# Performance work log

Measured on AMD Instinct MI355X. Metric: run time of the kernel, lower is better.

Reference implementation:

```python
import jax, jax.numpy as jnp
import numpy as np

C = 512
NC = 12
EPS = 1e-5

ADJ = np.array([
    [0,0,0,1,0,1,1,1,1,1,1,1],
    [0,0,0,1,0,1,1,1,1,1,1,1],
    [0,0,0,1,0,1,1,1,1,1,1,1],
    [1,1,1,0,1,1,1,1,1,1,1,1],
    [0,0,0,1,0,1,1,1,1,1,1,1],
    [1,1,1,1,1,0,1,1,1,0,0,0],
    [1,1,1,1,1,1,0,0,0,1,1,1],
    [1,1,1,1,1,1,0,0,0,1,1,1],
    [1,1,1,1,1,1,0,0,0,1,1,1],
    [1,1,1,1,1,0,1,1,1,0,0,0],
    [1,1,1,1,1,0,1,1,1,0,0,0],
    [1,1,1,1,1,0,1,1,1,0,0,0]], dtype=np.float32)
# per-AU region selection: 0=up,1=mid,2=down1,3=down2 (AU1,2,4 up; AU6 mid; AU7 up; AU10 d2; AU12,14,15 d1; AU17,23,24 d2)
SEL = np.array([0,0,0,1,0,3,2,2,2,3,3,3])


def setup_inputs() -> dict:
    key = jax.random.key(0)
    ks = jax.random.split(key, 12)
    B, T = 32, 32
    BT = B * T
    s = (2.0 / C) ** 0.5
    return {
        'x': jax.random.normal(ks[0], (BT, 49, C), jnp.float32),
        'adj_mask': jnp.ones((BT, NC, NC), jnp.float32),
        'region_W': jax.random.normal(ks[1], (4, C, C), jnp.float32) * s,
        'region_b': jnp.zeros((4, C), jnp.float32),
        'region_gamma': jnp.ones((4, C), jnp.float32),
        'region_beta': jnp.zeros((4, C), jnp.float32),
        'upfc_W': jax.random.normal(ks[2], (C, 16), jnp.float32) * 0.02,
        'upfc_b': jnp.zeros((16,), jnp.float32),
        'midfc_W': jax.random.normal(ks[3], (C, 2), jnp.float32) * 0.02,
        'midfc_b': jnp.zeros((2,), jnp.float32),
        'd1fc_W': jax.random.normal(ks[4], (C, 8), jnp.float32) * 0.02,
        'd1fc_b': jnp.zeros((8,), jnp.float32),
        'd2fc_W': jax.random.normal(ks[5], (C, 16), jnp.float32) * 0.02,
        'd2fc_b': jnp.zeros((16,), jnp.float32),
        'class_W': jax.random.normal(ks[6], (NC, C, C), jnp.float32) * s,
        'class_b': jnp.zeros((NC, C), jnp.float32),
        'class_gamma': jnp.ones((NC, C), jnp.float32),
        'class_beta': jnp.zeros((NC, C), jnp.float32),
        'gat_W': jax.random.normal(ks[7], (C, C), jnp.float32) * 0.02,
        'gat_al': jax.random.normal(ks[8], (C,), jnp.float32) * 0.02,
        'gat_ar': jax.random.normal(ks[9], (C,), jnp.float32) * 0.02,
        'tconv_W': jax.random.normal(ks[10], (NC, C, 5), jnp.float32) * 0.1,
        'tconv_b': jnp.zeros((NC, C), jnp.float32),
        'tbn_gamma': jnp.ones((NC,), jnp.float32),
        'tbn_beta': jnp.zeros((NC,), jnp.float32),
        'B': B,
        'T': T,
    }


def _bn(x, gamma, beta, axes):
    # training-mode batch norm: stats over `axes`, affine per remaining channel
    mean = x.mean(axes, keepdims=True)
    var = x.var(axes, keepdims=True)
    return gamma * (x - mean) * jax.lax.rsqrt(var + EPS) + beta


def reference(x, adj_mask, region_W, region_b, region_gamma, region_beta,
              upfc_W, upfc_b, midfc_W, midfc_b, d1fc_W, d1fc_b, d2fc_W, d2fc_b,
              class_W, class_b, class_gamma, class_beta,
              gat_W, gat_al, gat_ar, tconv_W, tconv_b, tbn_gamma, tbn_beta, B, T):
    BT = x.shape[0]
    xg = x.reshape(BT, 7, 7, C)
    x_up = xg[:, :3].reshape(BT, 21, C)
    x_mid = xg[:, 2:5].reshape(BT, 21, C)
    x_down = xg[:, 4:].reshape(BT, 21, C)
    # 4 region LinearBlocks (fc -> BN over (batch,seq) per channel -> relu), batched
    regions = jnp.stack([x_up, x_mid, x_down, x_down])  # [4,BT,21,C]
    h = jnp.einsum('rbsc,rcd->rbsd', regions, region_W) + region_b[:, None, None, :]
    h = jax.nn.relu(_bn(h, region_gamma[:, None, None, :], region_beta[:, None, None, :], (1, 2)))
    up_pred = h[0].mean(1) @ upfc_W + upfc_b
    mid_pred = h[1].mean(1) @ midfc_W + midfc_b
    d1_pred = h[2].mean(1) @ d1fc_W + d1fc_b
    d2_pred = h[3].mean(1) @ d2fc_W + d2fc_b
    # 12 per-AU LinearBlocks, batched over the class dim
    cls_in = h[jnp.asarray(SEL)]  # [12,BT,21,C]
    y = jnp.einsum('nbsc,ncd->nbsd', cls_in, class_W) + class_b[:, None, None, :]
    y = jax.nn.relu(_bn(y, class_gamma[:, None, None, :], class_beta[:, None, None, :], (1, 2)))
    f_v = y.mean(2).transpose(1, 0, 2)  # [BT,12,C]
    # cross-region single-head GAT over the fixed 12-node graph, residual, thred=0.1
    adj = jnp.asarray(ADJ)[None] * adj_mask + jnp.eye(NC, dtype=x.dtype)
    hg = f_v @ gat_W  # [BT,12,C]
    e = jax.nn.leaky_relu((hg @ gat_al)[:, :, None] + (hg @ gat_ar)[:, None, :], 0.2)
    attn = jax.nn.softmax(jnp.where(adj > 0.1, e, -1e9), axis=-1)
    g = jnp.einsum('bij,bjc->bic', attn, hg) + f_v
    # per-class depthwise temporal Conv1d (k=5, pad=2, groups=C), batched over classes
    x4 = g.reshape(B, T, NC, C)
    xp = jnp.pad(x4, ((0, 0), (2, 2), (0, 0), (0, 0)))
    v = sum(xp[:, k:k + T] * tconv_W[None, None, :, :, k] for k in range(5)) + tconv_b[None, None]
    v = v.reshape(BT, NC, C)
    out = jax.nn.relu(_bn(v, tbn_gamma[None, :, None], tbn_beta[None, :, None], (0, 2)))
    return (up_pred, mid_pred, d1_pred, d2_pred, out)
```

## Files before the change

### kernel.cpp

```cpp
#include <hip/hip_runtime.h>
#include <hip/hip_bf16.h>

typedef unsigned short u16;
typedef __attribute__((ext_vector_type(8))) __bf16 bf16x8;
typedef __attribute__((ext_vector_type(8))) u16 u16x8;
typedef __attribute__((ext_vector_type(4))) float floatx4;

#define C_     512
#define NC_    12
#define BT_    1024
#define SEQ_   21
#define M_REG  21504
#define M_GAT  12288

__device__ __forceinline__ float bf2f(u16 u) {
  unsigned int v = ((unsigned int)u) << 16;
  float f; __builtin_memcpy(&f, &v, 4); return f;
}
__device__ __forceinline__ u16 f2bf(float f) {
  unsigned int b; __builtin_memcpy(&b, &f, 4);
  unsigned int r = (b + 0x7FFFu + ((b >> 16) & 1u)) >> 16;
  return (u16)r;
}
__device__ __forceinline__ float ldf(const void* p, size_t i, int f32) {
  return f32 ? ((const float*)p)[i] : bf2f(((const u16*)p)[i]);
}
__device__ __forceinline__ u16 ldbf(const void* p, size_t i, int f32) {
  return f32 ? f2bf(((const float*)p)[i]) : ((const u16*)p)[i];
}
__device__ __forceinline__ void stout(void* p, size_t i, float v, int f32) {
  if (f32) ((float*)p)[i] = v; else ((u16*)p)[i] = f2bf(v);
}

typedef __attribute__((address_space(1))) unsigned int as1_u32;
typedef __attribute__((address_space(3))) unsigned int as3_u32;
__device__ __forceinline__ void gl2lds16(const void* g, void* l) {
  __builtin_amdgcn_global_load_lds((const as1_u32*)g, (as3_u32*)l, 16, 0, 0);
}

__global__ void sent_k(float* __restrict__ o, float val) {
  const int i = blockIdx.x * 256 + threadIdx.x;
  if (i < 16384) o[i] = val;
}

__global__ void detect_k(const u16* __restrict__ x, int* __restrict__ flag) {
  __shared__ int cnt;
  if (threadIdx.x == 0) cnt = 0;
  __syncthreads();
  int bad = 0;
  for (int i = threadIdx.x; i < 4096; i += 256) {
    const float v = bf2f(x[i]);
    const float a = fabsf(v);
    if (!(a <= 1e4f)) bad++;
    else if (a > 0.f && a < 1e-35f) bad++;
  }
  atomicAdd(&cnt, bad);
  __syncthreads();
  if (threadIdx.x == 0) *flag = (cnt > 400) ? 1 : 0;
}

__global__ void zero_stats(float* __restrict__ p, int n) {
  const int id = blockIdx.x * 256 + threadIdx.x;
  if (id < n) p[id] = 0.f;
}

__global__ void transpose512(const void* __restrict__ rW, const void* __restrict__ cW,
                             const void* __restrict__ gW, u16* __restrict__ oR,
                             u16* __restrict__ oC, u16* __restrict__ oG,
                             const int* __restrict__ flagp) {
  const int f32 = *flagp;
  const int z = blockIdx.z;
  const void* src; u16* dst; size_t sofs = 0;
  if (z < 4)       { src = rW; sofs = (size_t)z*262144;     dst = oR + (size_t)z*262144; }
  else if (z < 16) { src = cW; sofs = (size_t)(z-4)*262144; dst = oC + (size_t)(z-4)*262144; }
  else             { src = gW;                              dst = oG; }
  __shared__ u16 t[32][33];
  const int tx = threadIdx.x;
  const int cy = blockIdx.y * 32, dx = blockIdx.x * 32;
  for (int i = threadIdx.y; i < 32; i += 8)
    t[i][tx] = ldbf(src, sofs + (size_t)(cy + i)*512 + dx + tx, f32);
  __syncthreads();
  for (int i = threadIdx.y; i < 32; i += 8)
    dst[(size_t)(dx + i)*512 + cy + tx] = t[tx][i];
}

template<int MODE>
__global__ __launch_bounds__(256)
void gemm_k(const void* __restrict__ Abase, const u16* __restrict__ Wtb,
            const void* __restrict__ biasb, u16* __restrict__ outb,
            float* __restrict__ ssumb, float* __restrict__ ssqb,
            const int* __restrict__ flagp, int pk, int n0)
{
  const int f32 = *flagp;
  const int z = blockIdx.z;
  const int zeff = (MODE == 1) ? (n0 + z) : z;
  const void* A = Abase;
  if (MODE == 1) A = (const void*)((const u16*)Abase +
        (size_t)((pk >> (zeff * 2)) & 3) * ((size_t)M_REG * C_));
  const u16* Wt = Wtb + (size_t)zeff * C_ * C_;
  u16* Out = outb + (size_t)z * (size_t)M_REG * C_;

  __shared__ __align__(16) u16 smem[64 * 132];
  u16* As = smem;
  u16* Bs = smem + 4096;

  const int tid  = threadIdx.x;
  const int w    = tid >> 6;
  const int lane = tid & 63;
  const int wm   = w >> 1, wn = w & 1;
  const int r16  = lane & 15, q = lane >> 4;

  const int band = (MODE == 2) ? 12 : 21;
  const int lin  = blockIdx.x;
  const int xcd  = lin & 7;
  const int idx  = lin >> 3;
  const int mi   = xcd * band + idx % band;
  const int ni   = idx / band;
  const int m0   = mi * 128;
  const int nn0  = ni * 128;

  const int sub = lane >> 2;
  const int kq  = (lane & 3) * 8;
  const int am0 = m0 + w*32 + sub;
  const int am1 = am0 + 16;
  long ga0, ga1;
  if (MODE == 0) {
    const int roff = (pk >> (z * 8)) & 0xFF;
    int q21 = am0 / 21; int rm = am0 - q21*21;
    ga0 = (long)q21*49 + roff + rm;
    q21 = am1 / 21; rm = am1 - q21*21;
    ga1 = (long)q21*49 + roff + rm;
  } else { ga0 = am0; ga1 = am1; }
  const size_t aOff0 = (size_t)ga0 * C_ + kq;
  const size_t aOff1 = (size_t)ga1 * C_ + kq;
  const u16* bSrc0 = Wt + (size_t)(nn0 + w*32 + sub) * C_ + kq;
  const u16* bSrc1 = bSrc0 + (size_t)16 * C_;
  u16* aDstW0 = &As[(w*32 +  0) * 32];
  u16* aDstW1 = &As[(w*32 + 16) * 32];
  u16* bDstW0 = &Bs[(w*32 +  0) * 32];
  u16* bDstW1 = &Bs[(w*32 + 16) * 32];
  u16x8* aLds0 = (u16x8*)&As[(w*32 + sub +  0) * 32 + kq];
  u16x8* aLds1 = (u16x8*)&As[(w*32 + sub + 16) * 32 + kq];

  floatx4 acc[4][4];
  #pragma unroll
  for (int i = 0; i < 4; i++)
    #pragma unroll
    for (int j = 0; j < 4; j++)
      acc[i][j] = (floatx4){0.f, 0.f, 0.f, 0.f};

  for (int kk = 0; kk < C_; kk += 32) {
    if (MODE == 0 && f32) {
      const float* p0 = (const float*)A + aOff0 + kk;
      const float* p1 = (const float*)A + aOff1 + kk;
      const floatx4 f00 = *(const floatx4*)p0;
      const floatx4 f01 = *(const floatx4*)(p0 + 4);
      const floatx4 f10 = *(const floatx4*)p1;
      const floatx4 f11 = *(const floatx4*)(p1 + 4);
      u16x8 va0, va1;
      #pragma unroll
      for (int j = 0; j < 4; j++) {
        va0[j] = f2bf(f00[j]); va0[4+j] = f2bf(f01[j]);
        va1[j] = f2bf(f10[j]); va1[4+j] = f2bf(f11[j]);
      }
      __syncthreads();
      gl2lds16(bSrc0, bDstW0); gl2lds16(bSrc1, bDstW1);
      *aLds0 = va0; *aLds1 = va1;
      __syncthreads();
    } else {
      __syncthreads();
      gl2lds16((const u16*)A + aOff0 + kk, aDstW0);
      gl2lds16((const u16*)A + aOff1 + kk, aDstW1);
      gl2lds16(bSrc0, bDstW0);
      gl2lds16(bSrc1, bDstW1);
      __syncthreads();
    }
    bSrc0 += 32; bSrc1 += 32;
    bf16x8 av[4], bv[4];
    #pragma unroll
    for (int mt = 0; mt < 4; mt++)
      av[mt] = *(const bf16x8*)&As[(wm*64 + mt*16 + r16)*32 + q*8];
    #pragma unroll
    for (int nt = 0; nt < 4; nt++)
      bv[nt] = *(const bf16x8*)&Bs[(wn*64 + nt*16 + r16)*32 + q*8];
    #pragma unroll
    for (int mt = 0; mt < 4; mt++)
      #pragma unroll
      for (int nt = 0; nt < 4; nt++)
        acc[mt][nt] = __builtin_amdgcn_mfma_f32_16x16x32_bf16(av[mt], bv[nt], acc[mt][nt], 0, 0, 0);
  }

  #pragma unroll
  for (int rh = 0; rh < 2; rh++) {
    __syncthreads();
    if (wm == rh) {
      #pragma unroll
      for (int nt = 0; nt < 4; nt++) {
        const int lcol = wn*64 + nt*16 + r16;
        float bvv = 0.f;
        if (MODE != 2) bvv = ldf(biasb, (size_t)zeff * C_ + nn0 + lcol, f32);
        float s = 0.f, s2 = 0.f;
        #pragma unroll
        for (int mt = 0; mt < 4; mt++) {
          #pragma unroll
          for (int p = 0; p < 4; p++) {
            const float v = acc[mt][nt][p] + bvv;
            s += v; s2 += v*v;
            smem[(mt*16 + q*4 + p)*132 + lcol] = f2bf(v);
          }
        }
        if (MODE != 2) {
          s  += __shfl_xor(s, 16);  s  += __shfl_xor(s, 32);
          s2 += __shfl_xor(s2, 16); s2 += __shfl_xor(s2, 32);
          if (q == 0) {
            atomicAdd(&ssumb[(size_t)zeff * C_ + nn0 + lcol], s);
            atomicAdd(&ssqb [(size_t)zeff * C_ + nn0 + lcol], s2);
          }
        }
      }
    }
    __syncthreads();
    #pragma unroll
    for (int rr = 0; rr < 4; rr++) {
      const int rl = rr*16 + (tid >> 4);
      const int cc = (tid & 15) * 8;
      const u16x8 vv = *(const u16x8*)&smem[rl*132 + cc];
      u16x8* dst = (u16x8*)&Out[(size_t)(m0 + rh*64 + rl) * C_ + nn0 + cc];
      if (MODE == 1) __builtin_nontemporal_store(vv, dst);
      else           *dst = vv;
    }
  }
}

__global__ void bn_region(u16* __restrict__ h, float* __restrict__ hbar,
                          const void* __restrict__ gamma, const void* __restrict__ beta,
                          const float* __restrict__ rsum, const float* __restrict__ rsq,
                          const int* __restrict__ flagp) {
  const int f32 = *flagp;
  const int gid  = blockIdx.x;
  const int r    = gid >> 8;
  const int bt   = ((gid & 255) << 2) + (threadIdx.x >> 6);
  const int lane = threadIdx.x & 63;
  const int d0   = lane * 8;
  const int rd   = r*512 + d0;
  float sc[8], sh[8], accv[8];
  #pragma unroll
  for (int j = 0; j < 8; j++) {
    const float mean = rsum[rd+j] * (1.f/21504.f);
    const float var  = fmaxf(rsq[rd+j] * (1.f/21504.f) - mean*mean, 0.f);
    sc[j] = ldf(gamma, rd+j, f32) * rsqrtf(var + 1e-5f);
    sh[j] = ldf(beta,  rd+j, f32) - mean * sc[j];
    accv[j] = 0.f;
  }
  const size_t base = ((size_t)r * M_REG + (size_t)bt * SEQ_) * C_ + d0;
  #pragma unroll
  for (int s = 0; s < SEQ_; s++) {
    u16x8 vv = *(u16x8*)&h[base + (size_t)s*C_];
    #pragma unroll
    for (int j = 0; j < 8; j++) {
      float v = fmaxf(sc[j] * bf2f(vv[j]) + sh[j], 0.f);
      vv[j] = f2bf(v);
      accv[j] += v;
    }
    *(u16x8*)&h[base + (size_t)s*C_] = vv;
  }
  float* hb = &hbar[((size_t)r * BT_ + bt) * C_ + d0];
  #pragma unroll
  for (int j = 0; j < 8; j++) hb[j] = accv[j] * (1.f/21.f);
}

__global__ void preds_k(const float* __restrict__ hbar,
                        const void* __restrict__ upW,  const void* __restrict__ upB,
                        const void* __restrict__ midW, const void* __restrict__ midB,
                        const void* __restrict__ d1W,  const void* __restrict__ d1B,
                        const void* __restrict__ d2W,  const void* __restrict__ d2B,
                        void* __restrict__ dout, const int* __restrict__ flagp) {
  const int f32 = *flagp;
  const int bt = blockIdx.x;
  __shared__ float hl[4][512];
  for (int i = threadIdx.x; i < 2048; i += 256)
    hl[i >> 9][i & 511] = hbar[((size_t)(i >> 9) * BT_ + bt) * C_ + (i & 511)];
  __syncthreads();
  const int j = threadIdx.x;
  if (j < 42) {
    int r, wdt, col; const void *W, *Bv; size_t oofs;
    if (j < 16)      { r=0; W=upW;  Bv=upB;  wdt=16; col=j;    oofs = (size_t)bt*16 + col; }
    else if (j < 18) { r=1; W=midW; Bv=midB; wdt=2;  col=j-16; oofs = 16384 + (size_t)bt*2 + col; }
    else if (j < 26) { r=2; W=d1W;  Bv=d1B;  wdt=8;  col=j-18; oofs = 18432 + (size_t)bt*8 + col; }
    else             { r=3; W=d2W;  Bv=d2B;  wdt=16; col=j-26; oofs = 26624 + (size_t)bt*16 + col; }
    float acc = ldf(Bv, col, f32);
    for (int d = 0; d < 512; d++) acc += hl[r][d] * ldf(W, d*wdt + col, f32);
    stout(dout, oofs, acc, f32);
  }
}

__global__ void bn_class_mean(const u16* __restrict__ ypre, u16* __restrict__ fv,
                              const void* __restrict__ gamma, const void* __restrict__ beta,
                              const float* __restrict__ csum, const float* __restrict__ csq,
                              const int* __restrict__ flagp, int n0) {
  const int f32 = *flagp;
  const int gid  = blockIdx.x;
  const int zz   = gid >> 8;
  const int bt   = ((gid & 255) << 2) + (threadIdx.x >> 6);
  const int lane = threadIdx.x & 63;
  const int d0   = lane * 8;
  const int n    = n0 + zz;
  const int nd   = n*512 + d0;
  float sc[8], sh[8], accv[8];
  #pragma unroll
  for (int j = 0; j < 8; j++) {
    const float mean = csum[nd+j] * (1.f/21504.f);
    const float var  = fmaxf(csq[nd+j] * (1.f/21504.f) - mean*mean, 0.f);
    sc[j] = ldf(gamma, nd+j, f32) * rsqrtf(var + 1e-5f);
    sh[j] = ldf(beta,  nd+j, f32) - mean * sc[j];
    accv[j] = 0.f;
  }
  const size_t base = ((size_t)zz * M_REG + (size_t)bt * SEQ_) * C_ + d0;
  #pragma unroll
  for (int s = 0; s < SEQ_; s++) {
    const u16x8 vv = __builtin_nontemporal_load((const u16x8*)&ypre[base + (size_t)s*C_]);
    #pragma unroll
    for (int j = 0; j < 8; j++)
      accv[j] += fmaxf(sc[j] * bf2f(vv[j]) + sh[j], 0.f);
  }
  u16x8 ov;
  #pragma unroll
  for (int j = 0; j < 8; j++) ov[j] = f2bf(accv[j] * (1.f/21.f));
  *(u16x8*)&fv[((size_t)bt * NC_ + n) * C_ + d0] = ov;
}

__global__ __launch_bounds__(256)
void gat_k(const u16* __restrict__ hg, const u16* __restrict__ fv,
           const void* __restrict__ al, const void* __restrict__ ar,
           const void* __restrict__ adj_mask, float* __restrict__ g,
           const int* __restrict__ flagp) {
  const int f32 = *flagp;
  const int bt = blockIdx.x;
  __shared__ float hl[12][512];
  __shared__ float alv[12], arv[12], attn[12][12];
  const u16* hgb = hg + (size_t)bt * NC_ * C_;
  for (int i = threadIdx.x; i < 6144; i += 256)
    hl[i >> 9][i & 511] = bf2f(hgb[i]);
  __syncthreads();
  const int w = threadIdx.x >> 6, lane = threadIdx.x & 63;
  for (int i = w; i < 12; i += 4) {
    float pa = 0.f, pr = 0.f;
    #pragma unroll
    for (int jj = 0; jj < 8; jj++) {
      const int c = lane*8 + jj;
      const float hv = hl[i][c];
      pa += hv * ldf(al, c, f32);
      pr += hv * ldf(ar, c, f32);
    }
    #pragma unroll
    for (int off = 32; off; off >>= 1) { pa += __shfl_xor(pa, off); pr += __shfl_xor(pr, off); }
    if (lane == 0) { alv[i] = pa; arv[i] = pr; }
  }
  __syncthreads();
  if (threadIdx.x < 12) {
    const unsigned AM[12] = {0xFE8,0xFE8,0xFE8,0xFF7,0xFE8,0x1DF,
                             0xE3F,0xE3F,0xE3F,0x1DF,0x1DF,0x1DF};
    const int i = threadIdx.x;
    float row[12]; float mx = -1e30f;
    #pragma unroll
    for (int jx = 0; jx < 12; jx++) {
      const float maskv = ldf(adj_mask, (size_t)bt*144 + i*12 + jx, f32);
      const float adjv = (float)((AM[i] >> jx) & 1u) * maskv + (i == jx ? 1.f : 0.f);
      float e;
      if (adjv > 0.1f) {
        const float t = alv[i] + arv[jx];
        e = t > 0.f ? t : 0.2f * t;
      } else e = -1e9f;
      row[jx] = e; mx = fmaxf(mx, e);
    }
    float den = 0.f;
    #pragma unroll
    for (int jx = 0; jx < 12; jx++) { const float ex = __expf(row[jx] - mx); row[jx] = ex; den += ex; }
    const float inv = 1.f / den;
    #pragma unroll
    for (int jx = 0; jx < 12; jx++) attn[i][jx] = row[jx] * inv;
  }
  __syncthreads();
  const u16* fvb = fv + (size_t)bt * NC_ * C_;
  float* gb = g + (size_t)bt * NC_ * C_;
  for (int o = threadIdx.x; o < 6144; o += 256) {
    const int i = o >> 9, c = o & 511;
    float acc = bf2f(fvb[o]);
    #pragma unroll
    for (int jx = 0; jx < 12; jx++) acc += attn[i][jx] * hl[jx][c];
    gb[o] = acc;
  }
}

__global__ void tconv_k(float* __restrict__ g, const void* __restrict__ tw,
                        const void* __restrict__ tb, float* __restrict__ tsum,
                        float* __restrict__ tsq, const int* __restrict__ flagp) {
  const int f32 = *flagp;
  const int id = blockIdx.x * 256 + threadIdx.x;
  const int c = id & 511;
  const int n = (id >> 9) % 12;
  const int b = id / 6144;
  float wk[5];
  #pragma unroll
  for (int k = 0; k < 5; k++) wk[k] = ldf(tw, (size_t)(n*512 + c)*5 + k, f32);
  const float bias = ldf(tb, n*512 + c, f32);
  float xv[36];
  xv[0] = xv[1] = xv[34] = xv[35] = 0.f;
  const size_t base = ((size_t)b * 32 * NC_ + n) * C_ + c;
  #pragma unroll
  for (int t = 0; t < 32; t++) xv[t + 2] = g[base + (size_t)t * 6144];
  float s = 0.f, s2 = 0.f;
  float ov[32];
  #pragma unroll
  for (int t = 0; t < 32; t++) {
    float v = bias;
    #pragma unroll
    for (int k = 0; k < 5; k++) v += wk[k] * xv[t + k];
    ov[t] = v; s += v; s2 += v*v;
  }
  #pragma unroll
  for (int t = 0; t < 32; t++) g[base + (size_t)t * 6144] = ov[t];
  #pragma unroll
  for (int off = 32; off; off >>= 1) { s += __shfl_xor(s, off); s2 += __shfl_xor(s2, off); }
  if ((threadIdx.x & 63) == 0) { atomicAdd(&tsum[n], s); atomicAdd(&tsq[n], s2); }
}

__global__ void bn_t(const float* __restrict__ v, void* __restrict__ outp,
                     const void* __restrict__ tg, const void* __restrict__ tb2,
                     const float* __restrict__ tsum, const float* __restrict__ tsq,
                     const int* __restrict__ flagp) {
  const int f32 = *flagp;
  const size_t id = (size_t)blockIdx.x * 256 + threadIdx.x;
  const int n = (int)((id >> 9) % 12);
  const float mean = tsum[n] * (1.f/524288.f);
  const float var  = fmaxf(tsq[n] * (1.f/524288.f) - mean*mean, 0.f);
  const float sc = ldf(tg, n, f32) * rsqrtf(var + 1e-5f);
  const float sh = ldf(tb2, n, f32) - mean * sc;
  stout(outp, 43008 + id, fmaxf(sc * v[id] + sh, 0.f), f32);
}

static constexpr size_t OFF_FLAG = 0;
static constexpr size_t OFF_STAT = 64;
static constexpr int    STAT_N   = 2048+2048+6144+6144+12+12;
static constexpr size_t OFF_WTR  = 65792;
static constexpr size_t OFF_WTC  = OFF_WTR + (size_t)4*512*512*2;
static constexpr size_t OFF_WTG  = OFF_WTC + (size_t)12*512*512*2;
static constexpr size_t OFF_H    = OFF_WTG + (size_t)512*512*2;
static constexpr size_t OFF_HBAR = OFF_H + (size_t)4*M_REG*C_*2;
static constexpr size_t OFF_FV   = OFF_HBAR + (size_t)4*BT_*C_*4;
static constexpr size_t OFF_AREN = OFF_FV + (size_t)M_GAT*C_*2;
static constexpr size_t YPRE_B   = (size_t)M_REG * C_ * 2;
static constexpr size_t NEEDED   = OFF_AREN + YPRE_B;

extern "C" void kernel_launch(void* const* d_in, const int* in_sizes, int n_in,
                              void* d_out, int out_size, void* d_ws, size_t ws_size,
                              hipStream_t stream) {
  const u16* x        = (const u16*)d_in[0];
  const void* adj_m   = d_in[1];
  const void* region_W= d_in[2];
  const void* region_b= d_in[3];
  const void* region_g= d_in[4];
  const void* region_be=d_in[5];
  const void* upW  = d_in[6];   const void* upB  = d_in[7];
  const void* midW = d_in[8];   const void* midB = d_in[9];
  const void* d1W  = d_in[10];  const void* d1B  = d_in[11];
  const void* d2W  = d_in[12];  const void* d2B  = d_in[13];
  const void* class_W = d_in[14];
  const void* class_b = d_in[15];
  const void* class_g = d_in[16];
  const void* class_be= d_in[17];
  const void* gat_W   = d_in[18];
  const void* gat_al  = d_in[19];
  const void* gat_ar  = d_in[20];
  const void* tconv_W = d_in[21];
  const void* tconv_b = d_in[22];
  const void* tbn_g   = d_in[23];
  const void* tbn_be  = d_in[24];

  char* ws = (char*)d_ws;
  int*   flagp = (int*)(ws + OFF_FLAG);
  float* rsum = (float*)(ws + OFF_STAT);
  float* rsq  = rsum + 2048;
  float* csum = rsq  + 2048;
  float* csq  = csum + 6144;
  float* tsum = csq  + 6144;
  float* tsq  = tsum + 12;
  u16*   WtR  = (u16*)(ws + OFF_WTR);
  u16*   WtC  = (u16*)(ws + OFF_WTC);
  u16*   WtG  = (u16*)(ws + OFF_WTG);
  u16*   h    = (u16*)(ws + OFF_H);
  float* hbar = (float*)(ws + OFF_HBAR);
  u16*   fv   = (u16*)(ws + OFF_FV);
  u16*   ypre = (u16*)(ws + OFF_AREN);
  u16*   hg   = (u16*)(ws + OFF_AREN);
  float* g    = (float*)(ws + OFF_H);

  int errStage = 0, errCode = 0;
  (void)hipGetLastError();
  #define CK(s) do { hipError_t e_ = hipGetLastError(); \
      if (e_ != hipSuccess && errStage == 0) { errStage = (s); errCode = (int)e_; } } while(0)

  sent_k<<<64, 256, 0, stream>>>((float*)d_out, 50.f); CK(12);

  if (ws_size < NEEDED) {
    int mb = (int)(ws_size >> 20); if (mb > 999) mb = 999;
    sent_k<<<64, 256, 0, stream>>>((float*)d_out, 13000.f + (float)mb);
    return;
  }

  int nch = (int)((ws_size - OFF_AREN) / YPRE_B);
  if (nch > 12) nch = 12;
  if (nch < 1) nch = 1;

  const int ROFFPACK = 0 | (14 << 8) | (28 << 16) | (28 << 24);
  const int SELPACK  = (1 << 6) | (3 << 10) | (2 << 12) | (2 << 14) |
                       (2 << 16) | (3 << 18) | (3 << 20) | (3 << 22);

  detect_k<<<1, 256, 0, stream>>>(x, flagp);                         CK(1);
  zero_stats<<<(STAT_N + 255)/256, 256, 0, stream>>>(rsum, STAT_N);  CK(1);
  transpose512<<<dim3(16,16,17), dim3(32,8), 0, stream>>>(
      region_W, class_W, gat_W, WtR, WtC, WtG, flagp);               CK(2);

  gemm_k<0><<<dim3(672,1,4), 256, 0, stream>>>(
      x, WtR, region_b, h, rsum, rsq, flagp, ROFFPACK, 0);           CK(3);
  bn_region<<<1024, 256, 0, stream>>>(h, hbar, region_g, region_be,
      rsum, rsq, flagp);                                             CK(4);
  preds_k<<<1024, 256, 0, stream>>>(hbar, upW,upB, midW,midB,
      d1W,d1B, d2W,d2B, d_out, flagp);                               CK(5);

  for (int n0 = 0; n0 < 12; n0 += nch) {
    const int zc = (12 - n0) < nch ? (12 - n0) : nch;
    gemm_k<1><<<dim3(672,1,zc), 256, 0, stream>>>(
        h, WtC, class_b, ypre, csum, csq, flagp, SELPACK, n0);       CK(6);
    bn_class_mean<<<zc*256, 256, 0, stream>>>(ypre, fv, class_g, class_be,
        csum, csq, flagp, n0);                                       CK(7);
  }

  gemm_k<2><<<dim3(384,1,1), 256, 0, stream>>>(
      fv, WtG, nullptr, hg, nullptr, nullptr, flagp, 0, 0);          CK(8);
  gat_k<<<1024, 256, 0, stream>>>(hg, fv, gat_al, gat_ar, adj_m, g, flagp); CK(9);
  tconv_k<<<768, 256, 0, stream>>>(g, tconv_W, tconv_b, tsum, tsq, flagp);  CK(10);
  bn_t<<<24576, 256, 0, stream>>>(g, d_out, tbn_g, tbn_be, tsum, tsq, flagp); CK(11);

  if (errStage) {
    int ec = errCode > 999 ? 999 : errCode;
    sent_k<<<64, 256, 0, stream>>>((float*)d_out, (float)(errStage*1000 + ec));
  }
  #undef CK
}
```

Measured before the change: 798.2 us.

## Vectorize small kernels, merge detect and zero-stats, parallelize preds reduction

Several independent small-kernel tweaks. The flag-detection and stats-zeroing kernels are merged into one launch. preds_k now splits each dot product across a wavefront with a shuffle reduction instead of one thread looping over 512 elements. gat_k and bn_t switch to vectorized loads and stores, with bn_t launching a quarter of the blocks. bn_class_mean drops its nontemporal load hint. These target launch overhead and serial or scalar memory access in the minor kernels, while the GEMMs that dominate runtime are left unchanged.

Result: no change. 786.2 us (-1.5%).

```diff
diff --git a/kernel.cpp b/kernel.cpp
--- a/kernel.cpp
+++ b/kernel.cpp
@@ -4,6 +4,7 @@
 typedef unsigned short u16;
 typedef __attribute__((ext_vector_type(8))) __bf16 bf16x8;
 typedef __attribute__((ext_vector_type(8))) u16 u16x8;
+typedef __attribute__((ext_vector_type(4))) u16 u16x4;
 typedef __attribute__((ext_vector_type(4))) float floatx4;
 
 #define C_     512
@@ -43,25 +44,26 @@
   if (i < 16384) o[i] = val;
 }
 
-__global__ void detect_k(const u16* __restrict__ x, int* __restrict__ flag) {
-  __shared__ int cnt;
-  if (threadIdx.x == 0) cnt = 0;
-  __syncthreads();
-  int bad = 0;
-  for (int i = threadIdx.x; i < 4096; i += 256) {
-    const float v = bf2f(x[i]);
-    const float a = fabsf(v);
-    if (!(a <= 1e4f)) bad++;
-    else if (a > 0.f && a < 1e-35f) bad++;
-  }
-  atomicAdd(&cnt, bad);
-  __syncthreads();
-  if (threadIdx.x == 0) *flag = (cnt > 400) ? 1 : 0;
-}
-
-__global__ void zero_stats(float* __restrict__ p, int n) {
-  const int id = blockIdx.x * 256 + threadIdx.x;
-  if (id < n) p[id] = 0.f;
+__global__ void detect_k(const u16* __restrict__ x, int* __restrict__ flag,
+                         float* __restrict__ stats, int nstat) {
+  if (blockIdx.x == 0) {
+    __shared__ int cnt;
+    if (threadIdx.x == 0) cnt = 0;
+    __syncthreads();
+    int bad = 0;
+    for (int i = threadIdx.x; i < 4096; i += 256) {
+      const float v = bf2f(x[i]);
+      const float a = fabsf(v);
+      if (!(a <= 1e4f)) bad++;
+      else if (a > 0.f && a < 1e-35f) bad++;
+    }
+    atomicAdd(&cnt, bad);
+    __syncthreads();
+    if (threadIdx.x == 0) *flag = (cnt > 400) ? 1 : 0;
+  } else {
+    const int id = (blockIdx.x - 1) * 256 + threadIdx.x;
+    if (id < nstat) stats[id] = 0.f;
+  }
 }
 
 __global__ void transpose512(const void* __restrict__ rW, const void* __restrict__ cW,
@@ -281,16 +283,22 @@
   for (int i = threadIdx.x; i < 2048; i += 256)
     hl[i >> 9][i & 511] = hbar[((size_t)(i >> 9) * BT_ + bt) * C_ + (i & 511)];
   __syncthreads();
-  const int j = threadIdx.x;
-  if (j < 42) {
+  const int w = threadIdx.x >> 6, lane = threadIdx.x & 63;
+  for (int j = w; j < 42; j += 4) {
     int r, wdt, col; const void *W, *Bv; size_t oofs;
     if (j < 16)      { r=0; W=upW;  Bv=upB;  wdt=16; col=j;    oofs = (size_t)bt*16 + col; }
     else if (j < 18) { r=1; W=midW; Bv=midB; wdt=2;  col=j-16; oofs = 16384 + (size_t)bt*2 + col; }
     else if (j < 26) { r=2; W=d1W;  Bv=d1B;  wdt=8;  col=j-18; oofs = 18432 + (size_t)bt*8 + col; }
     else             { r=3; W=d2W;  Bv=d2B;  wdt=16; col=j-26; oofs = 26624 + (size_t)bt*16 + col; }
-    float acc = ldf(Bv, col, f32);
-    for (int d = 0; d < 512; d++) acc += hl[r][d] * ldf(W, d*wdt + col, f32);
-    stout(dout, oofs, acc, f32);
+    float acc = 0.f;
+    #pragma unroll
+    for (int e = 0; e < 8; e++) {
+      const int d = lane*8 + e;
+      acc += hl[r][d] * ldf(W, (size_t)d*wdt + col, f32);
+    }
+    #pragma unroll
+    for (int off = 32; off; off >>= 1) acc += __shfl_xor(acc, off);
+    if (lane == 0) stout(dout, oofs, acc + ldf(Bv, col, f32), f32);
   }
 }
 
@@ -318,7 +326,7 @@
   const size_t base = ((size_t)zz * M_REG + (size_t)bt * SEQ_) * C_ + d0;
   #pragma unroll
   for (int s = 0; s < SEQ_; s++) {
-    const u16x8 vv = __builtin_nontemporal_load((const u16x8*)&ypre[base + (size_t)s*C_]);
+    const u16x8 vv = *(const u16x8*)&ypre[base + (size_t)s*C_];
     #pragma unroll
     for (int j = 0; j < 8; j++)
       accv[j] += fmaxf(sc[j] * bf2f(vv[j]) + sh[j], 0.f);
@@ -339,8 +347,12 @@
   __shared__ float hl[12][512];
   __shared__ float alv[12], arv[12], attn[12][12];
   const u16* hgb = hg + (size_t)bt * NC_ * C_;
-  for (int i = threadIdx.x; i < 6144; i += 256)
-    hl[i >> 9][i & 511] = bf2f(hgb[i]);
+  for (int i = threadIdx.x * 8; i < 6144; i += 2048) {
+    const u16x8 vv = *(const u16x8*)&hgb[i];
+    const int ii = i >> 9, cc = i & 511;
+    #pragma unroll
+    for (int e = 0; e < 8; e++) hl[ii][cc + e] = bf2f(vv[e]);
+  }
   __syncthreads();
   const int w = threadIdx.x >> 6, lane = threadIdx.x & 63;
   for (int i = w; i < 12; i += 4) {
@@ -430,13 +442,24 @@
                      const float* __restrict__ tsum, const float* __restrict__ tsq,
                      const int* __restrict__ flagp) {
   const int f32 = *flagp;
-  const size_t id = (size_t)blockIdx.x * 256 + threadIdx.x;
-  const int n = (int)((id >> 9) % 12);
+  const size_t id4 = (size_t)blockIdx.x * 256 + threadIdx.x;
+  const int n = (int)((id4 >> 7) % 12);
   const float mean = tsum[n] * (1.f/524288.f);
   const float var  = fmaxf(tsq[n] * (1.f/524288.f) - mean*mean, 0.f);
   const float sc = ldf(tg, n, f32) * rsqrtf(var + 1e-5f);
   const float sh = ldf(tb2, n, f32) - mean * sc;
-  stout(outp, 43008 + id, fmaxf(sc * v[id] + sh, 0.f), f32);
+  const floatx4 vv = *(const floatx4*)&v[id4 * 4];
+  if (f32) {
+    floatx4 ov;
+    #pragma unroll
+    for (int e = 0; e < 4; e++) ov[e] = fmaxf(sc * vv[e] + sh, 0.f);
+    *(floatx4*)&((float*)outp)[43008 + id4*4] = ov;
+  } else {
+    u16x4 ov;
+    #pragma unroll
+    for (int e = 0; e < 4; e++) ov[e] = f2bf(fmaxf(sc * vv[e] + sh, 0.f));
+    *(u16x4*)&((u16*)outp)[43008 + id4*4] = ov;
+  }
 }
 
 static constexpr size_t OFF_FLAG = 0;
@@ -516,8 +539,7 @@
   const int SELPACK  = (1 << 6) | (3 << 10) | (2 << 12) | (2 << 14) |
                        (2 << 16) | (3 << 18) | (3 << 20) | (3 << 22);
 
-  detect_k<<<1, 256, 0, stream>>>(x, flagp);                         CK(1);
-  zero_stats<<<(STAT_N + 255)/256, 256, 0, stream>>>(rsum, STAT_N);  CK(1);
+  detect_k<<<1 + (STAT_N + 255)/256, 256, 0, stream>>>(x, flagp, rsum, STAT_N); CK(1);
   transpose512<<<dim3(16,16,17), dim3(32,8), 0, stream>>>(
       region_W, class_W, gat_W, WtR, WtC, WtG, flagp);               CK(2);
 
@@ -540,7 +562,7 @@
       fv, WtG, nullptr, hg, nullptr, nullptr, flagp, 0, 0);          CK(8);
   gat_k<<<1024, 256, 0, stream>>>(hg, fv, gat_al, gat_ar, adj_m, g, flagp); CK(9);
   tconv_k<<<768, 256, 0, stream>>>(g, tconv_W, tconv_b, tsum, tsq, flagp);  CK(10);
-  bn_t<<<24576, 256, 0, stream>>>(g, d_out, tbn_g, tbn_be, tsum, tsq, flagp); CK(11);
+  bn_t<<<6144, 256, 0, stream>>>(g, d_out, tbn_g, tbn_be, tsum, tsq, flagp); CK(11);
 
   if (errStage) {
     int ec = errCode > 999 ? 999 : errCode;
```
